# Optimization experiments

Measured on AMD Instinct MI355X. Metric: run time of the kernel, lower is better.

## Reference

```python
import jax, jax.numpy as jnp
import numpy as np

N = 8192          # number of signals (rows of Y)
DIM_BASIS = 512   # signal dimension n
NUM_BASIS = 2048  # dictionary atoms m (overcomplete)
SC_ITERS = 20     # FISTA iterations
PM_ITERS = 100    # power-method iterations


def setup_inputs() -> dict:
    key = jax.random.key(0)
    kY, kW = jax.random.split(key)
    Y = jax.random.normal(kY, (N, DIM_BASIS), jnp.float32)
    W = jax.random.normal(kW, (DIM_BASIS, NUM_BASIS), jnp.float32)
    # NormDict applied in __init__: unit-norm columns
    W = W / jnp.linalg.norm(W, axis=0, keepdims=True)
    K = jnp.asarray(0.1, jnp.float32)  # lamda for FISTA soft-threshold
    return {"Y": Y, "W": W, "K": K}


def _soft(x, lam):
    return jnp.sign(x) * jax.nn.relu(jnp.abs(x) - lam)


def _power_method(W):
    # largest eigenvalue of W^T W (W: [n, m]); fixed random init for determinism
    X0 = jax.random.normal(jax.random.key(1), (1, W.shape[1]), W.dtype)

    def body(i, carry):
        X, _ = carry
        X = (X @ W.T) @ W          # X <- X W^T W, shape [1, m]
        nm = jnp.linalg.norm(X)
        return (X / nm, nm)

    _, nm = jax.lax.fori_loop(0, PM_ITERS, body, (X0, jnp.asarray(1.0, W.dtype)))
    return nm


def _fista(Y, W, lam, iters):
    c = _power_method(W)
    eta = 1.0 / c
    Gamma0 = _soft(Y @ (eta * W), lam)     # [N, m]
    Yn = jnp.linalg.norm(Y)

    def step(carry, _):
        Gamma, Z, t = carry
        residual = Z @ W.T - Y                              # [N, n]
        Gamma_new = _soft(Z - eta * (residual @ W), lam / c)
        t_new = (1.0 + jnp.sqrt(1.0 + 4.0 * t * t)) / 2.0
        Z_new = Gamma_new + ((t - 1.0) / t_new) * (Gamma_new - Gamma)
        nrm = jnp.linalg.norm(residual) / Yn
        return (Gamma_new, Z_new, t_new), nrm

    init = (Gamma0, Gamma0, jnp.asarray(1.0, Y.dtype))
    (Gamma, _, _), norms = jax.lax.scan(step, init, None, length=iters)
    return Gamma, norms


def reference(Y, W, K):
    # NormDict at start of forward (done on .data in torch -> no grad through norm)
    Wn = W / jax.lax.stop_gradient(jnp.linalg.norm(W, axis=0, keepdims=True))
    # W.requires_grad_(False) during sparse coding
    W_ng = jax.lax.stop_gradient(Wn)
    Gamma, norms = _fista(Y, W_ng, K, SC_ITERS)
    X = Gamma @ Wn.T   # reconstruction, grad flows to W here only
    return X, Gamma, norms
```

## Files before the change

### kernel.cpp

```cpp
#include <hip/hip_runtime.h>
#include <cmath>

#define NR   8192
#define DB   512
#define NB   2048
#define ITERS 20
#define NSQ   9

typedef _Float16 hfrag_t __attribute__((ext_vector_type(8)));
typedef __attribute__((ext_vector_type(4))) float accv_t;
typedef unsigned short us4 __attribute__((ext_vector_type(4)));
typedef float f4 __attribute__((ext_vector_type(4)));

#define SL_Y2   0
#define SL_NUM  1
#define SL_DEN  2
#define SL_C    3
#define SL_ETA  4
#define SL_THR  5
#define SL_TR   6
#define SL_RES2 16

__device__ inline unsigned short f2h(float f) {
  _Float16 h = (_Float16)f;
  return __builtin_bit_cast(unsigned short, h);
}
__device__ inline float h2f(unsigned short u) {
  _Float16 h = __builtin_bit_cast(_Float16, u);
  return (float)h;
}
__device__ inline float softthr(float x, float t) {
  float a = fabsf(x) - t;
  return a > 0.f ? copysignf(a, x) : 0.f;
}


template<int MI, int NI, int NKT>
__device__ inline void gemm_tt(const unsigned short* __restrict__ At, int NTka,
                               const unsigned short* __restrict__ Bt, int NTkb,
                               int mt0, int nt0, accv_t acc[MI][NI]) {
  const int lane = threadIdx.x & 63;
  const int l16 = lane & 15, quad = lane >> 4;
  const int off = l16 * 16 + (quad & 1) * 8;
  const int kh = quad >> 1;
#pragma unroll
  for (int mi = 0; mi < MI; ++mi)
#pragma unroll
    for (int ni = 0; ni < NI; ++ni) acc[mi][ni] = (accv_t){0.f, 0.f, 0.f, 0.f};

#pragma unroll 4
  for (int kt = 0; kt < NKT; ++kt) {
    const int ktile = (kt << 1) + kh;
    hfrag_t af[MI], bf[NI];
#pragma unroll
    for (int mi = 0; mi < MI; ++mi)
      af[mi] = *(const hfrag_t*)&At[(((size_t)(mt0 + mi) * NTka + ktile) << 8) + off];
#pragma unroll
    for (int ni = 0; ni < NI; ++ni)
      bf[ni] = *(const hfrag_t*)&Bt[(((size_t)(nt0 + ni) * NTkb + ktile) << 8) + off];
#pragma unroll
    for (int mi = 0; mi < MI; ++mi)
#pragma unroll
      for (int ni = 0; ni < NI; ++ni)
        acc[mi][ni] = __builtin_amdgcn_mfma_f32_16x16x32_f16(bf[ni], af[mi], acc[mi][ni], 0, 0, 0);
  }
}

__device__ inline size_t ctile_off(int mt, int nt, int NTn) {
  int lane = threadIdx.x & 63;
  return (((size_t)mt * NTn + nt) << 8) + (lane & 15) * 16 + (lane >> 4) * 4;
}

__global__ void k_zero(float* slots) { if (threadIdx.x < 64) slots[threadIdx.x] = 0.f; }

__global__ void k_colnorm(const float* __restrict__ W, float* __restrict__ invn) {
  int j = blockIdx.x * 256 + threadIdx.x;
  float s = 0.f;
  for (int i = 0; i < DB; ++i) { float v = W[(size_t)i * NB + j]; s += v * v; }
  invn[j] = 1.0f / sqrtf(s);
}

__global__ void k_wnorm(const float* __restrict__ W, const float* __restrict__ invn,
                        unsigned short* __restrict__ Wn_t, unsigned short* __restrict__ Wt_t) {
  int tx = threadIdx.x & 31, ty = threadIdx.x >> 5;
  int j = blockIdx.x * 32 + tx;
  float inv = invn[j];
#pragma unroll
  for (int r = 0; r < 4; ++r) {
    int i = blockIdx.y * 32 + ty + r * 8;
    unsigned short h = f2h(W[(size_t)i * NB + j] * inv);
    Wn_t[(((size_t)(i >> 4) * (NB / 16) + (j >> 4)) << 8) + (i & 15) * 16 + (j & 15)] = h;
    Wt_t[(((size_t)(j >> 4) * (DB / 16) + (i >> 4)) << 8) + (j & 15) * 16 + (i & 15)] = h;
  }
}

__global__ void k_ynorm(const float* __restrict__ Y, unsigned short* __restrict__ Yh,
                        float* __restrict__ slots) {
  float s = 0.f;
  for (size_t u = (size_t)blockIdx.x * 256 + threadIdx.x; u < (size_t)(NR * DB / 4);
       u += (size_t)gridDim.x * 256) {
    int tile = (int)(u >> 6), r = (int)(u & 63);
    int mt = tile >> 5, nt = tile & 31;
    int m = mt * 16 + (r >> 2), n = nt * 16 + (r & 3) * 4;
    f4 v = *(const f4*)&Y[(size_t)m * DB + n];
    us4 h;
#pragma unroll
    for (int q = 0; q < 4; ++q) { h[q] = f2h(v[q]); s += v[q] * v[q]; }
    *(us4*)&Yh[u << 2] = h;
  }
  for (int off = 32; off > 0; off >>= 1) s += __shfl_xor(s, off);
  if ((threadIdx.x & 63) == 0) atomicAdd(&slots[SL_Y2], s);
}

__global__ __launch_bounds__(256) void k_sq(const float* __restrict__ S, float* __restrict__ D,
                                            const float* __restrict__ trIn, float* __restrict__ trOut) {
  __shared__ float tA[32][33], tB[32][33];
  int tx = threadIdx.x & 31, ty = threadIdx.x >> 5;
  int r0 = blockIdx.y * 32, c0 = blockIdx.x * 32;
  float inv = 1.0f / trIn[0];
  float acc[4] = {0.f, 0.f, 0.f, 0.f};
  for (int kt = 0; kt < 16; ++kt) {
    __syncthreads();
#pragma unroll
    for (int r = 0; r < 4; ++r) {
      tA[ty + r * 8][tx] = S[(size_t)(r0 + ty + r * 8) * DB + kt * 32 + tx];
      tB[ty + r * 8][tx] = S[(size_t)(kt * 32 + ty + r * 8) * DB + c0 + tx];
    }
    __syncthreads();
#pragma unroll
    for (int kk = 0; kk < 32; ++kk) {
      float b = tB[kk][tx];
#pragma unroll
      for (int r = 0; r < 4; ++r) acc[r] += tA[ty + r * 8][kk] * b;
    }
  }
  float inv2 = inv * inv;
#pragma unroll
  for (int r = 0; r < 4; ++r) {
    int row = r0 + ty + r * 8, col = c0 + tx;
    float v = acc[r] * inv2;
    D[(size_t)row * DB + col] = v;
    if (row == col) atomicAdd(trOut, v);
  }
}

__global__ void k_rayleigh(const float* __restrict__ Bm, const float* __restrict__ S,
                           float* __restrict__ slots) {
  int tid = blockIdx.x * 256 + threadIdx.x;
  float num = 0.f, den = 0.f;
  for (int i = tid; i < DB * DB; i += 256 * 256) {
    float s = S[i];
    num += Bm[i] * s;
    if ((i >> 9) == (i & 511)) den += s;
  }
  for (int off = 32; off > 0; off >>= 1) { num += __shfl_xor(num, off); den += __shfl_xor(den, off); }
  if ((threadIdx.x & 63) == 0) { atomicAdd(&slots[SL_NUM], num); atomicAdd(&slots[SL_DEN], den); }
}

__global__ void k_derive(float* slots, const float* __restrict__ Kp) {
  if (threadIdx.x == 0) {
    float cc = slots[SL_NUM] / slots[SL_DEN];
    slots[SL_C] = cc;
    float eta = 1.0f / cc;
    slots[SL_ETA] = eta;
    slots[SL_THR] = Kp[0] * eta;
  }
}

__global__ void k_norms(const float* __restrict__ slots, float* __restrict__ out) {
  int i = threadIdx.x;
  if (i < ITERS) out[i] = sqrtf(slots[SL_RES2 + i] / slots[SL_Y2]);
}

__global__ __launch_bounds__(256) void k_gemm_bbuild(const unsigned short* __restrict__ Wn_t,
                                                     float* __restrict__ Bm, float* __restrict__ slots) {
  accv_t acc[2][4];
  int w = threadIdx.x >> 6, lane = threadIdx.x & 63;
  int mt0 = blockIdx.y * 8 + w * 2, nt0 = blockIdx.x * 4;
  gemm_tt<2, 4, NB / 32>(Wn_t, NB / 16, Wn_t, NB / 16, mt0, nt0, acc);
  int l16 = lane & 15, quad = lane >> 4;
  float tr = 0.f;
#pragma unroll
  for (int mi = 0; mi < 2; ++mi)
#pragma unroll
    for (int ni = 0; ni < 4; ++ni) {
      int m = (mt0 + mi) * 16 + l16, nb = (nt0 + ni) * 16 + quad * 4;
      *(f4*)&Bm[(size_t)m * DB + nb] = acc[mi][ni];
#pragma unroll
      for (int r = 0; r < 4; ++r)
        if (m == nb + r) tr += acc[mi][ni][r];
    }
  if (tr != 0.f) atomicAdd(&slots[SL_TR], tr);
}

__global__ __launch_bounds__(256) void k_gemm_init(const unsigned short* __restrict__ Yh,
                                                   const unsigned short* __restrict__ Wt_t,
                                                   const float* __restrict__ slots,
                                                   const float* __restrict__ Kp,
                                                   unsigned short* __restrict__ Gh,
                                                   unsigned short* __restrict__ Zh) {
  accv_t acc[4][4];
  int w = threadIdx.x >> 6;
  int h = blockIdx.x;
  int xcd = h & 7, slot = h >> 3;
  int band = xcd * 8 + (slot >> 4);
  int nt = slot & 15;
  int mt0 = band * 8 + (w >> 1) * 4, nt0 = nt * 8 + (w & 1) * 4;
  gemm_tt<4, 4, DB / 32>(Yh, DB / 16, Wt_t, DB / 16, mt0, nt0, acc);
  float eta = slots[SL_ETA], lam = Kp[0];
#pragma unroll
  for (int mi = 0; mi < 4; ++mi)
#pragma unroll
    for (int ni = 0; ni < 4; ++ni) {
      size_t tb = ctile_off(mt0 + mi, nt0 + ni, NB / 16);
      us4 gq;
#pragma unroll
      for (int r = 0; r < 4; ++r) gq[r] = f2h(softthr(acc[mi][ni][r] * eta, lam));
      *(us4*)&Gh[tb] = gq;
      *(us4*)&Zh[tb] = gq;
    }
}

__global__ __launch_bounds__(256) void k_gemm_res(const unsigned short* __restrict__ Zh,
                                                  const unsigned short* __restrict__ Wn_t,
                                                  const unsigned short* __restrict__ Yh,
                                                  unsigned short* __restrict__ Rh,
                                                  float* __restrict__ res2slot) {
  accv_t acc[2][4];
  int w = threadIdx.x >> 6;
  int h = blockIdx.x;
  int xcd = h & 7, slot = h >> 3;
  int band = xcd * 8 + (slot >> 3);
  int nt = slot & 7;
  int mt0 = band * 8 + w * 2, nt0 = nt * 4;
  gemm_tt<2, 4, NB / 32>(Zh, NB / 16, Wn_t, NB / 16, mt0, nt0, acc);
  float s2 = 0.f;
#pragma unroll
  for (int mi = 0; mi < 2; ++mi)
#pragma unroll
    for (int ni = 0; ni < 4; ++ni) {
      size_t tb = ctile_off(mt0 + mi, nt0 + ni, DB / 16);
      us4 yq = *(const us4*)&Yh[tb];
      us4 rq;
#pragma unroll
      for (int r = 0; r < 4; ++r) {
        float rv = acc[mi][ni][r] - h2f(yq[r]);
        rq[r] = f2h(rv);
        s2 += rv * rv;
      }
      *(us4*)&Rh[tb] = rq;
    }
  for (int off = 32; off > 0; off >>= 1) s2 += __shfl_xor(s2, off);
  if ((threadIdx.x & 63) == 0) atomicAdd(res2slot, s2);
}

__global__ __launch_bounds__(256) void k_gemm_upd(const unsigned short* __restrict__ Rh,
                                                  const unsigned short* __restrict__ Wt_t,
                                                  const float* __restrict__ slots,
                                                  unsigned short* __restrict__ Gh,
                                                  unsigned short* __restrict__ Zh,
                                                  float* __restrict__ GammaOut,
                                                  float mom, int writeFinal) {
  accv_t acc[4][4];
  int w = threadIdx.x >> 6, lane = threadIdx.x & 63;
  int h = blockIdx.x;
  int xcd = h & 7, slot = h >> 3;
  int band = xcd * 8 + (slot >> 4);
  int nt = slot & 15;
  int mt0 = band * 8 + (w >> 1) * 4, nt0 = nt * 8 + (w & 1) * 4;
  gemm_tt<4, 4, DB / 32>(Rh, DB / 16, Wt_t, DB / 16, mt0, nt0, acc);
  int l16 = lane & 15, quad = lane >> 4;
  float eta = slots[SL_ETA], thr = slots[SL_THR];
#pragma unroll
  for (int mi = 0; mi < 4; ++mi)
#pragma unroll
    for (int ni = 0; ni < 4; ++ni) {
      size_t tb = ctile_off(mt0 + mi, nt0 + ni, NB / 16);
      us4 zq = *(const us4*)&Zh[tb];
      us4 gq = *(const us4*)&Gh[tb];
      us4 gho, zho;
      f4 gf;
#pragma unroll
      for (int r = 0; r < 4; ++r) {
        float z = h2f(zq[r]);
        float gold = h2f(gq[r]);
        float gn = softthr(z - eta * acc[mi][ni][r], thr);
        float zn = gn + mom * (gn - gold);
        gho[r] = f2h(gn);
        zho[r] = f2h(zn);
        gf[r] = gn;
      }
      *(us4*)&Gh[tb] = gho;
      *(us4*)&Zh[tb] = zho;
      if (writeFinal) {
        int m = (mt0 + mi) * 16 + l16, nb = (nt0 + ni) * 16 + quad * 4;
        *(f4*)&GammaOut[(size_t)m * NB + nb] = gf;
      }
    }
}

__global__ __launch_bounds__(256) void k_gemm_x(const unsigned short* __restrict__ Gh,
                                                const unsigned short* __restrict__ Wn_t,
                                                float* __restrict__ X) {
  accv_t acc[2][4];
  int w = threadIdx.x >> 6, lane = threadIdx.x & 63;
  int h = blockIdx.x;
  int xcd = h & 7, slot = h >> 3;
  int band = xcd * 8 + (slot >> 3);
  int nt = slot & 7;
  int mt0 = band * 8 + w * 2, nt0 = nt * 4;
  gemm_tt<2, 4, NB / 32>(Gh, NB / 16, Wn_t, NB / 16, mt0, nt0, acc);
  int l16 = lane & 15, quad = lane >> 4;
#pragma unroll
  for (int mi = 0; mi < 2; ++mi)
#pragma unroll
    for (int ni = 0; ni < 4; ++ni) {
      int m = (mt0 + mi) * 16 + l16, nb = (nt0 + ni) * 16 + quad * 4;
      *(f4*)&X[(size_t)m * DB + nb] = acc[mi][ni];
    }
}

extern "C" void kernel_launch(void* const* d_in, const int* in_sizes, int n_in,
                              void* d_out, int out_size, void* d_ws, size_t ws_size,
                              hipStream_t stream) {
  const float* Y  = (const float*)d_in[0];
  const float* W  = (const float*)d_in[1];
  const float* Kp = (const float*)d_in[2];

  float* Xout     = (float*)d_out;
  float* GammaOut = Xout + (size_t)NR * DB;
  float* NormsOut = GammaOut + (size_t)NR * NB;

  char* p = (char*)d_ws;
  auto carve = [&](size_t bytes) -> void* {
    void* r = (void*)p; p += (bytes + 255) & ~(size_t)255; return r;
  };
  float* slots = (float*)carve(64 * 4);
  float* invn  = (float*)carve(NB * 4);
  float* Bmat  = (float*)carve((size_t)DB * DB * 4);
  float* S0    = (float*)carve((size_t)DB * DB * 4);
  float* S1    = (float*)carve((size_t)DB * DB * 4);
  unsigned short* Wn_t = (unsigned short*)carve((size_t)DB * NB * 2);
  unsigned short* Wt_t = (unsigned short*)carve((size_t)NB * DB * 2);
  unsigned short* Yh   = (unsigned short*)carve((size_t)NR * DB * 2);
  unsigned short* Rh   = (unsigned short*)carve((size_t)NR * DB * 2);
  unsigned short* Zh   = (unsigned short*)carve((size_t)NR * NB * 2);
  unsigned short* Gh   = (unsigned short*)carve((size_t)NR * NB * 2);

  k_zero<<<1, 64, 0, stream>>>(slots);
  k_colnorm<<<NB / 256, 256, 0, stream>>>(W, invn);
  k_wnorm<<<dim3(NB / 32, DB / 32), 256, 0, stream>>>(W, invn, Wn_t, Wt_t);
  k_ynorm<<<1024, 256, 0, stream>>>(Y, Yh, slots);

  k_gemm_bbuild<<<dim3(DB / 64, DB / 128), 256, 0, stream>>>(Wn_t, Bmat, slots);
  float* ss[2] = {S0, S1};
  for (int k = 0; k < NSQ; ++k) {
    const float* in = (k == 0) ? Bmat : ss[(k + 1) & 1];
    k_sq<<<dim3(16, 16), 256, 0, stream>>>(in, ss[k & 1], slots + SL_TR + k, slots + SL_TR + k + 1);
  }
  k_rayleigh<<<256, 256, 0, stream>>>(Bmat, ss[(NSQ + 1) & 1], slots);
  k_derive<<<1, 64, 0, stream>>>(slots, Kp);

  k_gemm_init<<<1024, 256, 0, stream>>>(Yh, Wt_t, slots, Kp, Gh, Zh);
  double t = 1.0;
  for (int i = 0; i < ITERS; ++i) {
    k_gemm_res<<<512, 256, 0, stream>>>(Zh, Wn_t, Yh, Rh, slots + SL_RES2 + i);
    double tn = (1.0 + sqrt(1.0 + 4.0 * t * t)) / 2.0;
    float mom = (float)((t - 1.0) / tn);
    t = tn;
    k_gemm_upd<<<1024, 256, 0, stream>>>(Rh, Wt_t, slots, Gh, Zh, GammaOut,
                                         mom, (i == ITERS - 1) ? 1 : 0);
  }
  k_gemm_x<<<512, 256, 0, stream>>>(Gh, Wn_t, Xout);
  k_norms<<<1, 64, 0, stream>>>(slots, NormsOut);
}
```

Measured before the change: 2.484 ms.

## Split column-norm reduction, coalesce Y conversion, deepen GEMM unroll and set occupancy hints

The column-norm kernel is split across row blocks and accumulated with atomics, giving the old 8-block launch more parallelism. The Y-to-fp16 tiling kernel now reads full rows with 8-wide vectors and does one atomic per block. The long-K GEMMs (K=2048) unroll by 8 instead of 4, and the residual and X kernels get min-blocks-per-CU launch bounds. These target small setup-kernel latency and better latency hiding in the main GEMMs, at the risk of higher register pressure.

```diff
diff --git a/kernel.cpp b/kernel.cpp
--- a/kernel.cpp
+++ b/kernel.cpp
@@ -10,6 +10,7 @@
 typedef _Float16 hfrag_t __attribute__((ext_vector_type(8)));
 typedef __attribute__((ext_vector_type(4))) float accv_t;
 typedef unsigned short us4 __attribute__((ext_vector_type(4)));
+typedef unsigned short us8 __attribute__((ext_vector_type(8)));
 typedef float f4 __attribute__((ext_vector_type(4)));
 
 #define SL_Y2   0
@@ -35,7 +36,7 @@
 }
 
 
-template<int MI, int NI, int NKT>
+template<int MI, int NI, int NKT, int UNR>
 __device__ inline void gemm_tt(const unsigned short* __restrict__ At, int NTka,
                                const unsigned short* __restrict__ Bt, int NTkb,
                                int mt0, int nt0, accv_t acc[MI][NI]) {
@@ -48,8 +49,7 @@
 #pragma unroll
     for (int ni = 0; ni < NI; ++ni) acc[mi][ni] = (accv_t){0.f, 0.f, 0.f, 0.f};
 
-#pragma unroll 4
-  for (int kt = 0; kt < NKT; ++kt) {
+  auto kstep = [&](int kt) {
     const int ktile = (kt << 1) + kh;
     hfrag_t af[MI], bf[NI];
 #pragma unroll
@@ -63,6 +63,14 @@
 #pragma unroll
       for (int ni = 0; ni < NI; ++ni)
         acc[mi][ni] = __builtin_amdgcn_mfma_f32_16x16x32_f16(bf[ni], af[mi], acc[mi][ni], 0, 0, 0);
+  };
+
+  if constexpr (UNR == 8) {
+#pragma unroll 8
+    for (int kt = 0; kt < NKT; ++kt) kstep(kt);
+  } else {
+#pragma unroll 4
+    for (int kt = 0; kt < NKT; ++kt) kstep(kt);
   }
 }
 
@@ -71,20 +79,24 @@
   return (((size_t)mt * NTn + nt) << 8) + (lane & 15) * 16 + (lane >> 4) * 4;
 }
 
-__global__ void k_zero(float* slots) { if (threadIdx.x < 64) slots[threadIdx.x] = 0.f; }
-
-__global__ void k_colnorm(const float* __restrict__ W, float* __restrict__ invn) {
+__global__ void k_zero(float* slots, float* colsq) {
+  if (threadIdx.x < 64) slots[threadIdx.x] = 0.f;
+  for (int i = threadIdx.x; i < NB; i += 256) colsq[i] = 0.f;
+}
+
+__global__ void k_colsq(const float* __restrict__ W, float* __restrict__ colsq) {
   int j = blockIdx.x * 256 + threadIdx.x;
+  int r0 = blockIdx.y * 64;
   float s = 0.f;
-  for (int i = 0; i < DB; ++i) { float v = W[(size_t)i * NB + j]; s += v * v; }
-  invn[j] = 1.0f / sqrtf(s);
-}
-
-__global__ void k_wnorm(const float* __restrict__ W, const float* __restrict__ invn,
+  for (int i = 0; i < 64; ++i) { float v = W[(size_t)(r0 + i) * NB + j]; s += v * v; }
+  atomicAdd(&colsq[j], s);
+}
+
+__global__ void k_wnorm(const float* __restrict__ W, const float* __restrict__ colsq,
                         unsigned short* __restrict__ Wn_t, unsigned short* __restrict__ Wt_t) {
   int tx = threadIdx.x & 31, ty = threadIdx.x >> 5;
   int j = blockIdx.x * 32 + tx;
-  float inv = invn[j];
+  float inv = 1.0f / sqrtf(colsq[j]);
 #pragma unroll
   for (int r = 0; r < 4; ++r) {
     int i = blockIdx.y * 32 + ty + r * 8;
@@ -94,22 +106,30 @@
   }
 }
 
-__global__ void k_ynorm(const float* __restrict__ Y, unsigned short* __restrict__ Yh,
-                        float* __restrict__ slots) {
+__global__ __launch_bounds__(256) void k_ynorm(const float* __restrict__ Y,
+                                               unsigned short* __restrict__ Yh,
+                                               float* __restrict__ slots) {
+  __shared__ float part[4];
+  int w = threadIdx.x >> 6, lane = threadIdx.x & 63;
   float s = 0.f;
-  for (size_t u = (size_t)blockIdx.x * 256 + threadIdx.x; u < (size_t)(NR * DB / 4);
-       u += (size_t)gridDim.x * 256) {
-    int tile = (int)(u >> 6), r = (int)(u & 63);
-    int mt = tile >> 5, nt = tile & 31;
-    int m = mt * 16 + (r >> 2), n = nt * 16 + (r & 3) * 4;
-    f4 v = *(const f4*)&Y[(size_t)m * DB + n];
-    us4 h;
-#pragma unroll
-    for (int q = 0; q < 4; ++q) { h[q] = f2h(v[q]); s += v[q] * v[q]; }
-    *(us4*)&Yh[u << 2] = h;
+#pragma unroll
+  for (int rr = 0; rr < 4; ++rr) {
+    int m = blockIdx.x * 16 + w * 4 + rr;
+    const float* yrow = &Y[(size_t)m * DB + lane * 8];
+    f4 v0 = *(const f4*)yrow;
+    f4 v1 = *(const f4*)(yrow + 4);
+    us8 h;
+#pragma unroll
+    for (int q = 0; q < 4; ++q) {
+      h[q] = f2h(v0[q]);     s += v0[q] * v0[q];
+      h[4 + q] = f2h(v1[q]); s += v1[q] * v1[q];
+    }
+    *(us8*)&Yh[(((size_t)(m >> 4) * 32 + (lane >> 1)) << 8) + (m & 15) * 16 + (lane & 1) * 8] = h;
   }
   for (int off = 32; off > 0; off >>= 1) s += __shfl_xor(s, off);
-  if ((threadIdx.x & 63) == 0) atomicAdd(&slots[SL_Y2], s);
+  if (lane == 0) part[w] = s;
+  __syncthreads();
+  if (threadIdx.x == 0) atomicAdd(&slots[SL_Y2], part[0] + part[1] + part[2] + part[3]);
 }
 
 __global__ __launch_bounds__(256) void k_sq(const float* __restrict__ S, float* __restrict__ D,
@@ -172,12 +192,12 @@
   if (i < ITERS) out[i] = sqrtf(slots[SL_RES2 + i] / slots[SL_Y2]);
 }
 
-__global__ __launch_bounds__(256) void k_gemm_bbuild(const unsigned short* __restrict__ Wn_t,
-                                                     float* __restrict__ Bm, float* __restrict__ slots) {
+__global__ __launch_bounds__(256, 1) void k_gemm_bbuild(const unsigned short* __restrict__ Wn_t,
+                                                        float* __restrict__ Bm, float* __restrict__ slots) {
   accv_t acc[2][4];
   int w = threadIdx.x >> 6, lane = threadIdx.x & 63;
   int mt0 = blockIdx.y * 8 + w * 2, nt0 = blockIdx.x * 4;
-  gemm_tt<2, 4, NB / 32>(Wn_t, NB / 16, Wn_t, NB / 16, mt0, nt0, acc);
+  gemm_tt<2, 4, NB / 32, 8>(Wn_t, NB / 16, Wn_t, NB / 16, mt0, nt0, acc);
   int l16 = lane & 15, quad = lane >> 4;
   float tr = 0.f;
 #pragma unroll
@@ -206,7 +226,7 @@
   int band = xcd * 8 + (slot >> 4);
   int nt = slot & 15;
   int mt0 = band * 8 + (w >> 1) * 4, nt0 = nt * 8 + (w & 1) * 4;
-  gemm_tt<4, 4, DB / 32>(Yh, DB / 16, Wt_t, DB / 16, mt0, nt0, acc);
+  gemm_tt<4, 4, DB / 32, 4>(Yh, DB / 16, Wt_t, DB / 16, mt0, nt0, acc);
   float eta = slots[SL_ETA], lam = Kp[0];
 #pragma unroll
   for (int mi = 0; mi < 4; ++mi)
@@ -221,11 +241,11 @@
     }
 }
 
-__global__ __launch_bounds__(256) void k_gemm_res(const unsigned short* __restrict__ Zh,
-                                                  const unsigned short* __restrict__ Wn_t,
-                                                  const unsigned short* __restrict__ Yh,
-                                                  unsigned short* __restrict__ Rh,
-                                                  float* __restrict__ res2slot) {
+__global__ __launch_bounds__(256, 2) void k_gemm_res(const unsigned short* __restrict__ Zh,
+                                                     const unsigned short* __restrict__ Wn_t,
+                                                     const unsigned short* __restrict__ Yh,
+                                                     unsigned short* __restrict__ Rh,
+                                                     float* __restrict__ res2slot) {
   accv_t acc[2][4];
   int w = threadIdx.x >> 6;
   int h = blockIdx.x;
@@ -233,7 +253,7 @@
   int band = xcd * 8 + (slot >> 3);
   int nt = slot & 7;
   int mt0 = band * 8 + w * 2, nt0 = nt * 4;
-  gemm_tt<2, 4, NB / 32>(Zh, NB / 16, Wn_t, NB / 16, mt0, nt0, acc);
+  gemm_tt<2, 4, NB / 32, 8>(Zh, NB / 16, Wn_t, NB / 16, mt0, nt0, acc);
   float s2 = 0.f;
 #pragma unroll
   for (int mi = 0; mi < 2; ++mi)
@@ -268,7 +288,7 @@
   int band = xcd * 8 + (slot >> 4);
   int nt = slot & 15;
   int mt0 = band * 8 + (w >> 1) * 4, nt0 = nt * 8 + (w & 1) * 4;
-  gemm_tt<4, 4, DB / 32>(Rh, DB / 16, Wt_t, DB / 16, mt0, nt0, acc);
+  gemm_tt<4, 4, DB / 32, 4>(Rh, DB / 16, Wt_t, DB / 16, mt0, nt0, acc);
   int l16 = lane & 15, quad = lane >> 4;
   float eta = slots[SL_ETA], thr = slots[SL_THR];
 #pragma unroll
@@ -299,9 +319,9 @@
     }
 }
 
-__global__ __launch_bounds__(256) void k_gemm_x(const unsigned short* __restrict__ Gh,
-                                                const unsigned short* __restrict__ Wn_t,
-                                                float* __restrict__ X) {
+__global__ __launch_bounds__(256, 2) void k_gemm_x(const unsigned short* __restrict__ Gh,
+                                                   const unsigned short* __restrict__ Wn_t,
+                                                   float* __restrict__ X) {
   accv_t acc[2][4];
   int w = threadIdx.x >> 6, lane = threadIdx.x & 63;
   int h = blockIdx.x;
@@ -309,7 +329,7 @@
   int band = xcd * 8 + (slot >> 3);
   int nt = slot & 7;
   int mt0 = band * 8 + w * 2, nt0 = nt * 4;
-  gemm_tt<2, 4, NB / 32>(Gh, NB / 16, Wn_t, NB / 16, mt0, nt0, acc);
+  gemm_tt<2, 4, NB / 32, 8>(Gh, NB / 16, Wn_t, NB / 16, mt0, nt0, acc);
   int l16 = lane & 15, quad = lane >> 4;
 #pragma unroll
   for (int mi = 0; mi < 2; ++mi)
@@ -336,7 +356,7 @@
     void* r = (void*)p; p += (bytes + 255) & ~(size_t)255; return r;
   };
   float* slots = (float*)carve(64 * 4);
-  float* invn  = (float*)carve(NB * 4);
+  float* colsq = (float*)carve(NB * 4);
   float* Bmat  = (float*)carve((size_t)DB * DB * 4);
   float* S0    = (float*)carve((size_t)DB * DB * 4);
   float* S1    = (float*)carve((size_t)DB * DB * 4);
@@ -347,10 +367,10 @@
   unsigned short* Zh   = (unsigned short*)carve((size_t)NR * NB * 2);
   unsigned short* Gh   = (unsigned short*)carve((size_t)NR * NB * 2);
 
-  k_zero<<<1, 64, 0, stream>>>(slots);
-  k_colnorm<<<NB / 256, 256, 0, stream>>>(W, invn);
-  k_wnorm<<<dim3(NB / 32, DB / 32), 256, 0, stream>>>(W, invn, Wn_t, Wt_t);
-  k_ynorm<<<1024, 256, 0, stream>>>(Y, Yh, slots);
+  k_zero<<<1, 256, 0, stream>>>(slots, colsq);
+  k_colsq<<<dim3(NB / 256, DB / 64), 256, 0, stream>>>(W, colsq);
+  k_wnorm<<<dim3(NB / 32, DB / 32), 256, 0, stream>>>(W, colsq, Wn_t, Wt_t);
+  k_ynorm<<<512, 256, 0, stream>>>(Y, Yh, slots);
 
   k_gemm_bbuild<<<dim3(DB / 64, DB / 128), 256, 0, stream>>>(Wn_t, Bmat, slots);
   float* ss[2] = {S0, S1};
```

Result: slower. 2.594 ms (+4.4%).
